# Kernel optimization log

Measured on AMD Instinct MI355X. Metric: run time of the kernel, lower is better.

## Reference

```python
import jax, jax.numpy as jnp
import numpy as np

N_NODES = 5000
N_EDGES = 50000
BATCH = 8
SEQ = 12
IN_CH = 2
HID = 64
OUT_CH = 1
K = 3
N_LAYERS = 2


def setup_inputs() -> dict:
    key = jax.random.key(0)
    ks = jax.random.split(key, 20)
    d = {}
    d["x"] = jax.random.normal(ks[0], (BATCH, SEQ, N_NODES, IN_CH), dtype=jnp.float32)
    d["edge_index"] = jax.random.randint(ks[1], (2, N_EDGES), 0, N_NODES, dtype=jnp.int32)

    def w(k, fin):
        return jax.random.normal(k, (2, K, fin, HID), dtype=jnp.float32) * 0.05

    fins = [IN_CH + HID, HID + HID]
    i = 2
    for l in range(N_LAYERS):
        for g in ("z", "r", "h"):
            d["W" + g + str(l)] = w(ks[i], fins[l]); i += 1
            d["b" + g + str(l)] = jnp.zeros((HID,), jnp.float32)
    d["Wo"] = jax.random.normal(ks[i], (HID, OUT_CH), dtype=jnp.float32) * 0.05
    d["bo"] = jnp.zeros((OUT_CH,), jnp.float32)
    return d


def reference(x, edge_index,
              Wz0, bz0, Wr0, br0, Wh0, bh0,
              Wz1, bz1, Wr1, br1, Wh1, bh1,
              Wo, bo):
    B, T, N, _ = x.shape
    src, dst = edge_index[0], edge_index[1]
    ones = jnp.ones(src.shape, x.dtype)
    deg_out = jax.ops.segment_sum(ones, src, num_segments=N)
    deg_in = jax.ops.segment_sum(ones, dst, num_segments=N)
    inv = lambda dgr: jnp.where(dgr > 0, 1.0 / dgr, 0.0)
    norm_out = inv(deg_out)[src]  # [E], 1/deg_out(src)
    norm_in = inv(deg_in)[dst]    # [E], 1/deg_in(dst)

    def prop(X, norm):
        # X: [N, B, F] -> sparse matvec via gather/scatter
        msg = norm[:, None, None] * X[src]
        return jax.ops.segment_sum(msg, dst, num_segments=N)

    def dconv(X, W, b):
        # X: [N, B, Fin]; W: [2, K, Fin, H]; dual-direction Chebyshev diffusion
        H = jnp.einsum('nbf,fh->nbh', X, W[0, 0] + W[1, 0])
        Tx0o = Tx0i = X
        Tx1o = prop(X, norm_out)
        Tx1i = prop(X, norm_in)
        H = H + jnp.einsum('nbf,fh->nbh', Tx1o, W[0, 1]) \
              + jnp.einsum('nbf,fh->nbh', Tx1i, W[1, 1])
        for k in range(2, W.shape[1]):
            Tx2o = 2.0 * prop(Tx1o, norm_out) - Tx0o
            Tx2i = 2.0 * prop(Tx1i, norm_in) - Tx0i
            H = H + jnp.einsum('nbf,fh->nbh', Tx2o, W[0, k]) \
                  + jnp.einsum('nbf,fh->nbh', Tx2i, W[1, k])
            Tx0o, Tx1o = Tx1o, Tx2o
            Tx0i, Tx1i = Tx1i, Tx2i
        return H + b

    def cell(Xin, H, p):
        Wz, bz, Wr, br, Wh, bh = p
        XH = jnp.concatenate([Xin, H], axis=-1)
        Z = jax.nn.sigmoid(dconv(XH, Wz, bz))
        R = jax.nn.sigmoid(dconv(XH, Wr, br))
        Ht = jnp.tanh(dconv(jnp.concatenate([Xin, H * R], axis=-1), Wh, bh))
        return Z * H + (1.0 - Z) * Ht

    layers = [(Wz0, bz0, Wr0, br0, Wh0, bh0), (Wz1, bz1, Wr1, br1, Wh1, bh1)]
    hid = Wo.shape[0]
    h0 = jnp.zeros((len(layers), N, B, hid), x.dtype)
    xs = jnp.transpose(x, (1, 2, 0, 3))  # [T, N, B, F]

    def step(h, xt):
        inp = xt
        new_h = []
        for l, p in enumerate(layers):
            hl = cell(inp, h[l], p)
            new_h.append(hl)
            inp = hl
        h = jnp.stack(new_h)
        out = jnp.einsum('nbh,ho->nbo', h[-1], Wo) + bo
        return h, out

    _, outs = jax.lax.scan(step, h0, xs)      # [T, N, B, O]
    return jnp.transpose(outs, (2, 0, 1, 3))  # [B, T, N, O]
```

## Files before the change

### kernel.cpp

```cpp
#include <hip/hip_runtime.h>
#include <math.h>

#define NNODES 5000
#define NEDGES 50000
#define SEQT 12
#define NB 40000
#define MAXDEG 128

typedef __attribute__((ext_vector_type(8))) _Float16 half8;
typedef __attribute__((ext_vector_type(2))) _Float16 half2v;
typedef __attribute__((ext_vector_type(4))) float f32x4;


__global__ void count_deg_k(const int* __restrict__ ei, int* deg_out, int* deg_in){
    int e = blockIdx.x*blockDim.x + threadIdx.x;
    if (e < NEDGES){
        atomicAdd(&deg_out[ei[e]], 1);
        atomicAdd(&deg_in[ei[NEDGES + e]], 1);
    }
}

__global__ void scan_k(const int* __restrict__ deg_in, int* __restrict__ row_ptr){
    __shared__ int part[256];
    int tid = threadIdx.x;
    int base = tid*20;
    int loc[20]; int s = 0;
    for (int i=0;i<20;i++){
        int idx = base+i;
        int v = (idx < NNODES) ? deg_in[idx] : 0;
        loc[i] = s; s += v;
    }
    part[tid] = s;
    __syncthreads();
    for (int off=1; off<256; off<<=1){
        int v = (tid>=off) ? part[tid-off] : 0;
        __syncthreads();
        part[tid] += v;
        __syncthreads();
    }
    int prev = (tid==0) ? 0 : part[tid-1];
    for (int i=0;i<20;i++){
        int idx = base+i;
        if (idx < NNODES) row_ptr[idx] = prev + loc[i];
    }
    if (tid==255) row_ptr[NNODES] = part[255];
}

__global__ void fill_csr_k(const int* __restrict__ ei, const int* __restrict__ deg_out,
                           const int* __restrict__ deg_in, const int* __restrict__ row_ptr,
                           int* cursor, int* __restrict__ csr_src,
                           float* __restrict__ csr_wo, float* __restrict__ csr_wi){
    int e = blockIdx.x*blockDim.x + threadIdx.x;
    if (e >= NEDGES) return;
    int s = ei[e], d = ei[NEDGES+e];
    int pos = atomicAdd(&cursor[d], 1);
    int slot = row_ptr[d] + pos;
    csr_src[slot] = s;
    csr_wo[slot] = 1.f/(float)deg_out[s];
    csr_wi[slot] = 1.f/(float)deg_in[d];
}

__global__ void prepack_x_k(const float* __restrict__ x, _Float16* __restrict__ Xtph){
    int idx = blockIdx.x*256 + threadIdx.x;
    if (idx >= SEQT*NB*2) return;
    int tt = idx / (NB*2);
    int r2 = idx - tt*(NB*2);
    int row = r2 >> 1, f = r2 & 1;
    int n = row >> 3, b = row & 7;
    Xtph[idx] = (_Float16)x[((size_t)(b*SEQT+tt)*NNODES + n)*2 + f];
}

__device__ __forceinline__ float wfetch(const float* __restrict__ W, int F, int slot, int f, int c){
    const float* p0 = W + ((size_t)0*F + f)*64 + c;
    const float* p1 = W + ((size_t)1*F + f)*64 + c;
    const float* p2 = W + ((size_t)2*F + f)*64 + c;
    const float* p3 = W + ((size_t)3*F + f)*64 + c;
    const float* p4 = W + ((size_t)4*F + f)*64 + c;
    const float* p5 = W + ((size_t)5*F + f)*64 + c;
    switch(slot){
        case 0: return *p0 + *p3 - *p2 - *p5;
        case 1: return *p1;
        case 2: return *p4;
        case 3: return 2.f * *p2;
        default: return 2.f * *p5;
    }
}

__global__ void pack_l0_k(const float* __restrict__ W, _Float16* __restrict__ wh){
    int idx = blockIdx.x*256 + threadIdx.x;
    if (idx >= 4*11*64) return;
    int lane = idx & 63, rest = idx >> 6;
    int ks = rest % 11, cf = rest / 11;
    int col = cf*16 + (lane & 15);
    int kb = ks*32 + ((lane>>4)<<3);
    size_t o = ((size_t)(ks*4 + cf)*64 + lane)*8;
    for (int j=0;j<8;j++){
        int k = kb + j;
        float v = 0.f;
        if (ks == 0){
            if (k < 10) v = wfetch(W, 66, k>>1, k&1, col);
        } else {
            int slot = (ks-1)>>1;
            int f = 2 + k - 32 - 64*slot;
            v = wfetch(W, 66, slot, f, col);
        }
        wh[o+j] = (_Float16)v;
    }
}

__global__ void pack_l1_k(const float* __restrict__ W, _Float16* __restrict__ wh){
    int idx = blockIdx.x*256 + threadIdx.x;
    if (idx >= 4*20*64) return;
    int lane = idx & 63, rest = idx >> 6;
    int ks = rest % 20, cf = rest / 20;
    int col = cf*16 + (lane & 15);
    int kb = ks*32 + ((lane>>4)<<3);
    int slot = ks >> 2;
    size_t o = ((size_t)(ks*4 + cf)*64 + lane)*8;
    for (int j=0;j<8;j++){
        int k = kb + j;
        int f = k - slot*128;
        wh[o+j] = (_Float16)wfetch(W, 128, slot, f, col);
    }
}


__global__ __launch_bounds__(128) void k_f1(int aCount,
    const _Float16* __restrict__ h0h, const _Float16* __restrict__ h1h,
    _Float16* __restrict__ T1o128, _Float16* __restrict__ T1i128,
    const _Float16* __restrict__ Xt,
    _Float16* __restrict__ Th1o, _Float16* __restrict__ Th1i, _Float16* __restrict__ XTh,
    const int* __restrict__ rp, const int* __restrict__ cs,
    const float* __restrict__ cwo, const float* __restrict__ cwi){
    __shared__ int s_o[MAXDEG]; __shared__ float swo[MAXDEG], swi[MAXDEG];
    const int bx = blockIdx.x;
    const bool isA = bx < aCount;
    const int n = isA ? bx : bx - aCount;
    int beg = rp[n], deg = rp[n+1]-beg;
    int nst = deg < MAXDEG ? deg : MAXDEG;
    for (int j=threadIdx.x; j<nst; j+=128){
        s_o[j] = cs[beg+j]*512;
        swo[j] = cwo[beg+j]; swi[j] = cwi[beg+j];
    }
    __syncthreads();
    if (isA){
        int off = threadIdx.x*8;
        int b = off >> 7, c = off & 127;
        const _Float16* S = (c < 64) ? h0h : h1h;
        int soff = b*64 + (c & 63);
        float ao[8] = {0,0,0,0,0,0,0,0}, ai[8] = {0,0,0,0,0,0,0,0};
        for (int j=0;j<nst;j++){
            half8 v = *(const half8*)(S + s_o[j] + soff);
            float wo=swo[j], wi=swi[j];
            #pragma unroll
            for (int e=0;e<8;e++){
                float xv = (float)v[e];
                ao[e]=fmaf(wo,xv,ao[e]); ai[e]=fmaf(wi,xv,ai[e]);
            }
        }
        for (int j=nst;j<deg;j++){
            half8 v = *(const half8*)(S + (size_t)cs[beg+j]*512 + soff);
            float wo=cwo[beg+j], wi=cwi[beg+j];
            #pragma unroll
            for (int e=0;e<8;e++){
                float xv = (float)v[e];
                ao[e]=fmaf(wo,xv,ao[e]); ai[e]=fmaf(wi,xv,ai[e]);
            }
        }
        half8 po, pi;
        #pragma unroll
        for (int e=0;e<8;e++){ po[e]=(_Float16)ao[e]; pi[e]=(_Float16)ai[e]; }
        *(half8*)(T1o128 + (size_t)n*1024 + off) = po;
        *(half8*)(T1i128 + (size_t)n*1024 + off) = pi;
    } else {
        if (threadIdx.x < 64){
            int off = threadIdx.x*8;
            float ao[8] = {0,0,0,0,0,0,0,0}, ai[8] = {0,0,0,0,0,0,0,0};
            for (int j=0;j<nst;j++){
                half8 v = *(const half8*)(h0h + s_o[j] + off);
                float wo=swo[j], wi=swi[j];
                #pragma unroll
                for (int e=0;e<8;e++){
                    float xv = (float)v[e];
                    ao[e]=fmaf(wo,xv,ao[e]); ai[e]=fmaf(wi,xv,ai[e]);
                }
            }
            for (int j=nst;j<deg;j++){
                half8 v = *(const half8*)(h0h + (size_t)cs[beg+j]*512 + off);
                float wo=cwo[beg+j], wi=cwi[beg+j];
                #pragma unroll
                for (int e=0;e<8;e++){
                    float xv = (float)v[e];
                    ao[e]=fmaf(wo,xv,ao[e]); ai[e]=fmaf(wi,xv,ai[e]);
                }
            }
            half8 po, pi;
            #pragma unroll
            for (int e=0;e<8;e++){ po[e]=(_Float16)ao[e]; pi[e]=(_Float16)ai[e]; }
            *(half8*)(Th1o + (size_t)n*512 + off) = po;
            *(half8*)(Th1i + (size_t)n*512 + off) = pi;
        }
        if (threadIdx.x < 8){
            int b = threadIdx.x;
            float ax0=0,ax1=0, ay0=0,ay1=0;
            for (int j=0;j<nst;j++){
                int src = s_o[j] >> 9;
                half2v v = *(const half2v*)(Xt + src*16 + b*2);
                float x0=(float)v[0], x1=(float)v[1];
                ax0=fmaf(swo[j],x0,ax0); ax1=fmaf(swo[j],x1,ax1);
                ay0=fmaf(swi[j],x0,ay0); ay1=fmaf(swi[j],x1,ay1);
            }
            for (int j=nst;j<deg;j++){
                int src = cs[beg+j];
                half2v v = *(const half2v*)(Xt + src*16 + b*2);
                float x0=(float)v[0], x1=(float)v[1];
                ax0=fmaf(cwo[beg+j],x0,ax0); ax1=fmaf(cwo[beg+j],x1,ax1);
                ay0=fmaf(cwi[beg+j],x0,ay0); ay1=fmaf(cwi[beg+j],x1,ay1);
            }
            size_t ro = (size_t)(n*8 + b)*32;
            XTh[ro+0] = Xt[(size_t)(n*8+b)*2+0];
            XTh[ro+1] = Xt[(size_t)(n*8+b)*2+1];
            XTh[ro+2] = (_Float16)ax0; XTh[ro+3] = (_Float16)ax1;
            XTh[ro+4] = (_Float16)ay0; XTh[ro+5] = (_Float16)ay1;
        }
    }
}

__global__ __launch_bounds__(128) void k_f2(int aCount,
    const _Float16* __restrict__ T1o128, const _Float16* __restrict__ T1i128,
    _Float16* __restrict__ U2o128, _Float16* __restrict__ U2i128,
    const _Float16* __restrict__ Th1o, const _Float16* __restrict__ Th1i,
    _Float16* __restrict__ Th2o, _Float16* __restrict__ Th2i, _Float16* __restrict__ XTh,
    const int* __restrict__ rp, const int* __restrict__ cs,
    const float* __restrict__ cwo, const float* __restrict__ cwi){
    __shared__ int s_o[MAXDEG]; __shared__ float s_w[MAXDEG];
    const int bx = blockIdx.x;
    const bool isA = bx < aCount;
    const int idx = isA ? bx : bx - aCount;
    const int n = idx >> 1, sel = idx & 1;
    const float* cw = sel ? cwi : cwo;
    int beg = rp[n], deg = rp[n+1]-beg;
    int nst = deg < MAXDEG ? deg : MAXDEG;
    const int scale = isA ? 1024 : 512;
    for (int j=threadIdx.x; j<nst; j+=128){
        s_o[j] = cs[beg+j]*scale;
        s_w[j] = cw[beg+j];
    }
    __syncthreads();
    if (isA){
        const _Float16* S = sel ? T1i128 : T1o128;
        _Float16* U = sel ? U2i128 : U2o128;
        int off = threadIdx.x*8;
        float a[8] = {0,0,0,0,0,0,0,0};
        for (int j=0;j<nst;j++){
            half8 v = *(const half8*)(S + s_o[j] + off);
            float w=s_w[j];
            #pragma unroll
            for (int e=0;e<8;e++) a[e]=fmaf(w,(float)v[e],a[e]);
        }
        for (int j=nst;j<deg;j++){
            half8 v = *(const half8*)(S + (size_t)cs[beg+j]*1024 + off);
            float w=cw[beg+j];
            #pragma unroll
            for (int e=0;e<8;e++) a[e]=fmaf(w,(float)v[e],a[e]);
        }
        half8 p;
        #pragma unroll
        for (int e=0;e<8;e++) p[e]=(_Float16)a[e];
        *(half8*)(U + (size_t)n*1024 + off) = p;
    } else {
        const _Float16* S = sel ? Th1i : Th1o;
        _Float16* U = sel ? Th2i : Th2o;
        if (threadIdx.x < 64){
            int off = threadIdx.x*8;
            float a[8] = {0,0,0,0,0,0,0,0};
            for (int j=0;j<nst;j++){
                half8 v = *(const half8*)(S + s_o[j] + off);
                float w=s_w[j];
                #pragma unroll
                for (int e=0;e<8;e++) a[e]=fmaf(w,(float)v[e],a[e]);
            }
            for (int j=nst;j<deg;j++){
                half8 v = *(const half8*)(S + (size_t)cs[beg+j]*512 + off);
                float w=cw[beg+j];
                #pragma unroll
                for (int e=0;e<8;e++) a[e]=fmaf(w,(float)v[e],a[e]);
            }
            half8 p;
            #pragma unroll
            for (int e=0;e<8;e++) p[e]=(_Float16)a[e];
            *(half8*)(U + (size_t)n*512 + off) = p;
        }
        if (threadIdx.x < 8){
            int b = threadIdx.x;
            int xo = 2 + 2*sel;
            float a0=0,a1=0;
            for (int j=0;j<nst;j++){
                int src = s_o[j] >> 9;
                half2v v = *(const half2v*)(XTh + (size_t)src*256 + b*32 + xo);
                a0=fmaf(s_w[j],(float)v[0],a0); a1=fmaf(s_w[j],(float)v[1],a1);
            }
            for (int j=nst;j<deg;j++){
                int src = cs[beg+j];
                float w = cw[beg+j];
                half2v v = *(const half2v*)(XTh + (size_t)src*256 + b*32 + xo);
                a0=fmaf(w,(float)v[0],a0); a1=fmaf(w,(float)v[1],a1);
            }
            size_t ro = (size_t)(n*8 + b)*32 + 6 + 2*sel;
            XTh[ro+0] = (_Float16)a0; XTh[ro+1] = (_Float16)a1;
        }
    }
}

__global__ __launch_bounds__(64) void k_f4(int aCount,
    const _Float16* __restrict__ SA, _Float16* __restrict__ YoA, _Float16* __restrict__ YiA,
    const _Float16* __restrict__ SB, _Float16* __restrict__ YoB, _Float16* __restrict__ YiB,
    const int* __restrict__ rp, const int* __restrict__ cs,
    const float* __restrict__ cwo, const float* __restrict__ cwi){
    __shared__ int s_o[MAXDEG]; __shared__ float swo[MAXDEG], swi[MAXDEG];
    const int bx = blockIdx.x;
    const bool isA = bx < aCount;
    const int n = isA ? bx : bx - aCount;
    const _Float16* S = isA ? SA : SB;
    _Float16* Yo = isA ? YoA : YoB;
    _Float16* Yi = isA ? YiA : YiB;
    int beg = rp[n], deg = rp[n+1]-beg;
    int nst = deg < MAXDEG ? deg : MAXDEG;
    for (int j=threadIdx.x; j<nst; j+=64){
        s_o[j] = cs[beg+j]*512;
        swo[j] = cwo[beg+j]; swi[j] = cwi[beg+j];
    }
    __syncthreads();
    int off = threadIdx.x*8;
    float ao[8] = {0,0,0,0,0,0,0,0}, ai[8] = {0,0,0,0,0,0,0,0};
    for (int j=0;j<nst;j++){
        half8 v = *(const half8*)(S + s_o[j] + off);
        float wo=swo[j], wi=swi[j];
        #pragma unroll
        for (int e=0;e<8;e++){
            float xv = (float)v[e];
            ao[e]=fmaf(wo,xv,ao[e]); ai[e]=fmaf(wi,xv,ai[e]);
        }
    }
    for (int j=nst;j<deg;j++){
        half8 v = *(const half8*)(S + (size_t)cs[beg+j]*512 + off);
        float wo=cwo[beg+j], wi=cwi[beg+j];
        #pragma unroll
        for (int e=0;e<8;e++){
            float xv = (float)v[e];
            ao[e]=fmaf(wo,xv,ao[e]); ai[e]=fmaf(wi,xv,ai[e]);
        }
    }
    half8 po, pi;
    #pragma unroll
    for (int e=0;e<8;e++){ po[e]=(_Float16)ao[e]; pi[e]=(_Float16)ai[e]; }
    *(half8*)(Yo + (size_t)n*512 + off) = po;
    *(half8*)(Yi + (size_t)n*512 + off) = pi;
}

__global__ __launch_bounds__(64) void k_f5(int aCount,
    const _Float16* __restrict__ T1oA, const _Float16* __restrict__ T1iA,
    _Float16* __restrict__ U2oA, _Float16* __restrict__ U2iA,
    const _Float16* __restrict__ T1oB, const _Float16* __restrict__ T1iB,
    _Float16* __restrict__ U2oB, _Float16* __restrict__ U2iB,
    const int* __restrict__ rp, const int* __restrict__ cs,
    const float* __restrict__ cwo, const float* __restrict__ cwi){
    __shared__ int s_o[MAXDEG]; __shared__ float s_w[MAXDEG];
    const int bx = blockIdx.x;
    const bool isA = bx < aCount;
    const int idx = isA ? bx : bx - aCount;
    const int n = idx >> 1, sel = idx & 1;
    const _Float16* S = isA ? (sel ? T1iA : T1oA) : (sel ? T1iB : T1oB);
    _Float16* U = isA ? (sel ? U2iA : U2oA) : (sel ? U2iB : U2oB);
    const float* cw = sel ? cwi : cwo;
    int beg = rp[n], deg = rp[n+1]-beg;
    int nst = deg < MAXDEG ? deg : MAXDEG;
    for (int j=threadIdx.x; j<nst; j+=64){
        s_o[j] = cs[beg+j]*512;
        s_w[j] = cw[beg+j];
    }
    __syncthreads();
    int off = threadIdx.x*8;
    float a[8] = {0,0,0,0,0,0,0,0};
    for (int j=0;j<nst;j++){
        half8 v = *(const half8*)(S + s_o[j] + off);
        float w=s_w[j];
        #pragma unroll
        for (int e=0;e<8;e++) a[e]=fmaf(w,(float)v[e],a[e]);
    }
    for (int j=nst;j<deg;j++){
        half8 v = *(const half8*)(S + (size_t)cs[beg+j]*512 + off);
        float w=cw[beg+j];
        #pragma unroll
        for (int e=0;e<8;e++) a[e]=fmaf(w,(float)v[e],a[e]);
    }
    half8 p;
    #pragma unroll
    for (int e=0;e<8;e++) p[e]=(_Float16)a[e];
    *(half8*)(U + (size_t)n*512 + off) = p;
}


struct KD { const _Float16* a; int st; };
struct GA { KD kd[20]; };

template<int NK, int NG, int EPI>
__device__ __forceinline__ void gemm_body(char* smemraw, int bxm, const GA& ga,
    const _Float16* __restrict__ wh0, const float* __restrict__ b0,
    const _Float16* __restrict__ wh1, const float* __restrict__ b1,
    float* __restrict__ Z, _Float16* __restrict__ Gout,
    float* __restrict__ Hf, _Float16* __restrict__ Hh,
    const float* __restrict__ Wo, const float* __restrict__ bo,
    float* __restrict__ out, int t){
    _Float16* ldsb = (_Float16*)smemraw;
    float* spr = (float*)(smemraw + (size_t)4*NG*2048);
    const int tid = threadIdx.x;
    const int lane = tid & 63, wv = tid >> 6, rl = lane & 15, kg = lane >> 4;
    const int m0 = bxm*64 + (wv&1)*32;
    const int cfb = (wv>>1)*2;
    const _Float16* wsrc[2] = {wh0, wh1};

    half8 srg[NG];
    half8 a0, a1, a0n, a1n;

    auto sload = [&](int ks){
        #pragma unroll
        for (int j=0;j<NG;j++)
            srg[j] = *(const half8*)(wsrc[j] + (size_t)ks*2048 + tid*8);
    };
    auto swrite = [&](int buf){
        #pragma unroll
        for (int j=0;j<NG;j++)
            *(half8*)&ldsb[buf*(NG*2048) + j*2048 + tid*8] = srg[j];
    };
    auto aload = [&](int ks, half8& x0, half8& x1){
        const _Float16* base = ga.kd[ks].a;
        const int st = ga.kd[ks].st;
        x0 = *(const half8*)(base + (size_t)(m0+rl)*st + kg*8);
        x1 = *(const half8*)(base + (size_t)(m0+16+rl)*st + kg*8);
    };

    f32x4 acc[NG][2][2];
    #pragma unroll
    for (int g=0; g<NG; ++g)
        #pragma unroll
        for (int cc=0; cc<2; ++cc)
            #pragma unroll
            for (int mr=0; mr<2; ++mr){
                acc[g][cc][mr][0]=0.f; acc[g][cc][mr][1]=0.f;
                acc[g][cc][mr][2]=0.f; acc[g][cc][mr][3]=0.f;
            }

    sload(0); swrite(0);
    if (NK>1) sload(1);
    aload(0, a0, a1);
    __syncthreads();
    for (int ks=0; ks<NK; ++ks){
        const int cur = ks & 1;
        if (ks+1 < NK){ swrite(cur^1); aload(ks+1, a0n, a1n); }
        if (ks+2 < NK) sload(ks+2);
        #pragma unroll
        for (int g=0; g<NG; ++g){
            #pragma unroll
            for (int cc=0; cc<2; ++cc){
                half8 bv = *(const half8*)&ldsb[cur*(NG*2048) + g*2048 + (cfb+cc)*512 + lane*8];
                acc[g][cc][0] = __builtin_amdgcn_mfma_f32_16x16x32_f16(a0, bv, acc[g][cc][0], 0, 0, 0);
                acc[g][cc][1] = __builtin_amdgcn_mfma_f32_16x16x32_f16(a1, bv, acc[g][cc][1], 0, 0, 0);
            }
        }
        __syncthreads();
        a0 = a0n; a1 = a1n;
    }

    if constexpr (EPI == 0){
        #pragma unroll
        for (int cc=0; cc<2; ++cc){
            const int col = (cfb+cc)*16 + rl;
            float bzv = b0[col], brv = b1[col];
            #pragma unroll
            for (int mr=0; mr<2; ++mr)
                #pragma unroll
                for (int i=0;i<4;i++){
                    int row = m0 + mr*16 + kg*4 + i;
                    float z = 1.f/(1.f+__expf(-(acc[0][cc][mr][i] + bzv)));
                    float r = 1.f/(1.f+__expf(-(acc[NG-1][cc][mr][i] + brv)));
                    size_t ix = (size_t)row*64 + col;
                    Z[ix] = z;
                    Gout[ix] = (_Float16)(Hf[ix]*r);
                }
        }
    } else {
        float pr[2][4] = {{0.f,0.f,0.f,0.f},{0.f,0.f,0.f,0.f}};
        #pragma unroll
        for (int cc=0; cc<2; ++cc){
            const int col = (cfb+cc)*16 + rl;
            float bv = b0[col];
            float wo_c = 0.f;
            if constexpr (EPI == 2) wo_c = Wo[col];
            #pragma unroll
            for (int mr=0; mr<2; ++mr)
                #pragma unroll
                for (int i=0;i<4;i++){
                    int row = m0 + mr*16 + kg*4 + i;
                    float ht = tanhf(acc[0][cc][mr][i] + bv);
                    size_t ix = (size_t)row*64 + col;
                    float z = Z[ix];
                    float hn = z*Hf[ix] + (1.f-z)*ht;
                    Hf[ix] = hn;
                    Hh[ix] = (_Float16)hn;
                    if constexpr (EPI == 2) pr[mr][i] = fmaf(hn, wo_c, pr[mr][i]);
                }
        }
        if constexpr (EPI == 2){
            #pragma unroll
            for (int mr=0; mr<2; ++mr)
                #pragma unroll
                for (int i=0;i<4;i++){
                    float v = pr[mr][i];
                    v += __shfl_xor(v, 1);
                    v += __shfl_xor(v, 2);
                    v += __shfl_xor(v, 4);
                    v += __shfl_xor(v, 8);
                    if (rl == 0) spr[wv*32 + mr*16 + kg*4 + i] = v;
                }
            __syncthreads();
            if (tid < 64){
                int r = tid;
                float v = spr[(r>>5)*32 + (r&31)] + spr[((r>>5)|2)*32 + (r&31)] + bo[0];
                int row = bxm*64 + r;
                int n = row >> 3, b = row & 7;
                out[(size_t)(b*SEQT + t)*NNODES + n] = v;
            }
        }
    }
}

__global__ __launch_bounds__(256) void k_f3(int aCount,
    GA gaA, const _Float16* whA0, const float* bA0, const _Float16* whA1, const float* bA1,
    float* ZA, _Float16* GoA, float* HfA,
    GA gaB, const _Float16* whB0, const float* bB0, const _Float16* whB1, const float* bB1,
    float* ZB, _Float16* GoB, float* HfB){
    __shared__ __align__(16) char smem[4*2*2048 + 512];
    if (blockIdx.x < aCount)
        gemm_body<20,2,0>(smem, blockIdx.x, gaA, whA0, bA0, whA1, bA1,
                          ZA, GoA, HfA, nullptr, nullptr, nullptr, nullptr, 0);
    else
        gemm_body<11,2,0>(smem, blockIdx.x - aCount, gaB, whB0, bB0, whB1, bB1,
                          ZB, GoB, HfB, nullptr, nullptr, nullptr, nullptr, 0);
}

__global__ __launch_bounds__(256) void k_f6(int aCount,
    GA gaA, const _Float16* whA, const float* bA,
    float* ZA, float* HfA, _Float16* HhA,
    const float* Wo, const float* bo, float* out, int t,
    GA gaB, const _Float16* whB, const float* bB,
    float* ZB, float* HfB, _Float16* HhB){
    __shared__ __align__(16) char smem[4*1*2048 + 512];
    if (blockIdx.x < aCount)
        gemm_body<20,1,2>(smem, blockIdx.x, gaA, whA, bA, nullptr, nullptr,
                          ZA, nullptr, HfA, HhA, Wo, bo, out, t);
    else
        gemm_body<11,1,1>(smem, blockIdx.x - aCount, gaB, whB, bB, nullptr, nullptr,
                          ZB, nullptr, HfB, HhB, nullptr, nullptr, nullptr, 0);
}


extern "C" void kernel_launch(void* const* d_in, const int* in_sizes, int n_in,
                              void* d_out, int out_size, void* d_ws, size_t ws_size,
                              hipStream_t stream){
    (void)in_sizes; (void)n_in; (void)out_size; (void)ws_size;
    const float* x  = (const float*)d_in[0];
    const int*   ei = (const int*)d_in[1];
    const float* Wz[2] = {(const float*)d_in[2],  (const float*)d_in[8]};
    const float* bz[2] = {(const float*)d_in[3],  (const float*)d_in[9]};
    const float* Wr[2] = {(const float*)d_in[4],  (const float*)d_in[10]};
    const float* br[2] = {(const float*)d_in[5],  (const float*)d_in[11]};
    const float* Wh[2] = {(const float*)d_in[6],  (const float*)d_in[12]};
    const float* bh[2] = {(const float*)d_in[7],  (const float*)d_in[13]};
    const float* Wo = (const float*)d_in[14];
    const float* bo = (const float*)d_in[15];
    float* out = (float*)d_out;

    char* p = (char*)d_ws;
    auto alloc = [&](size_t bytes)->char*{
        char* r = p; p += (bytes + 255) & ~(size_t)255; return r;
    };
    const size_t H64  = (size_t)NB*64*2;
    const size_t H128 = (size_t)NB*128*2;
    const size_t F64  = (size_t)NB*64*4;

    _Float16* Xtph = (_Float16*)alloc((size_t)SEQT*NB*2*2);
    float*    h0f = (float*)alloc(F64);
    float*    h1f = (float*)alloc(F64);
    float*    Z0  = (float*)alloc(F64);
    float*    Z1  = (float*)alloc(F64);
    _Float16* h0hb[2];
    h0hb[0] = (_Float16*)alloc(H64);
    h0hb[1] = (_Float16*)alloc(H64);
    _Float16* h1h = (_Float16*)alloc(H64);
    _Float16* XTh = (_Float16*)alloc((size_t)NB*32*2);
    _Float16* Th1o = (_Float16*)alloc(H64);
    _Float16* Th1i = (_Float16*)alloc(H64);
    _Float16* Th2o = (_Float16*)alloc(H64);
    _Float16* Th2i = (_Float16*)alloc(H64);
    _Float16* G0L0 = (_Float16*)alloc(H64);
    _Float16* G1o0 = (_Float16*)alloc(H64);
    _Float16* G1i0 = (_Float16*)alloc(H64);
    _Float16* G2o0 = (_Float16*)alloc(H64);
    _Float16* G2i0 = (_Float16*)alloc(H64);
    _Float16* T1o128 = (_Float16*)alloc(H128);
    _Float16* T1i128 = (_Float16*)alloc(H128);
    _Float16* U2o128 = (_Float16*)alloc(H128);
    _Float16* U2i128 = (_Float16*)alloc(H128);
    _Float16* G0p  = (_Float16*)alloc(H64);
    _Float16* G1o1 = (_Float16*)alloc(H64);
    _Float16* G1i1 = (_Float16*)alloc(H64);
    _Float16* G2o1 = (_Float16*)alloc(H64);
    _Float16* G2i1 = (_Float16*)alloc(H64);
    _Float16 *whl0[3], *whl1[3];
    for (int g=0; g<3; ++g){
        whl0[g] = (_Float16*)alloc((size_t)4*11*64*8*2);
        whl1[g] = (_Float16*)alloc((size_t)4*20*64*8*2);
    }
    int* deg_out = (int*)alloc(NNODES*4);
    int* deg_in  = (int*)alloc(NNODES*4);
    int* row_ptr = (int*)alloc((NNODES+1)*4);
    int* cursor  = (int*)alloc(NNODES*4);
    int* csr_src = (int*)alloc(NEDGES*4);
    float* csr_wo = (float*)alloc(NEDGES*4);
    float* csr_wi = (float*)alloc(NEDGES*4);

    hipMemsetAsync(deg_out, 0, NNODES*4, stream);
    hipMemsetAsync(deg_in,  0, NNODES*4, stream);
    hipMemsetAsync(cursor,  0, NNODES*4, stream);
    hipMemsetAsync(h0f, 0, F64, stream);
    hipMemsetAsync(h1f, 0, F64, stream);
    hipMemsetAsync(h0hb[0], 0, H64, stream);
    hipMemsetAsync(h0hb[1], 0, H64, stream);
    hipMemsetAsync(h1h, 0, H64, stream);
    hipMemsetAsync(XTh, 0, (size_t)NB*32*2, stream);

    count_deg_k<<<(NEDGES+255)/256, 256, 0, stream>>>(ei, deg_out, deg_in);
    scan_k<<<1, 256, 0, stream>>>(deg_in, row_ptr);
    fill_csr_k<<<(NEDGES+255)/256, 256, 0, stream>>>(ei, deg_out, deg_in, row_ptr,
                                                     cursor, csr_src, csr_wo, csr_wi);
    prepack_x_k<<<(SEQT*NB*2+255)/256, 256, 0, stream>>>(x, Xtph);
    const float* Wptr0[3] = {Wz[0], Wr[0], Wh[0]};
    const float* Wptr1[3] = {Wz[1], Wr[1], Wh[1]};
    for (int g=0; g<3; ++g){
        pack_l0_k<<<(4*11*64+255)/256, 256, 0, stream>>>(Wptr0[g], whl0[g]);
        pack_l1_k<<<(4*20*64+255)/256, 256, 0, stream>>>(Wptr1[g], whl1[g]);
    }

    GA gaL0zr[2] = {}, gaL1zr[2] = {}, gaL1h[2] = {}, gaL0h = {};
    for (int pp=0; pp<2; ++pp){
        const _Float16* t64[5] = {h0hb[pp], Th1o, Th1i, Th2o, Th2i};
        gaL0zr[pp].kd[0] = {XTh, 32};
        for (int s=0; s<5; ++s){
            gaL0zr[pp].kd[1+2*s] = {t64[s], 64};
            gaL0zr[pp].kd[2+2*s] = {t64[s]+32, 64};
        }
        gaL1zr[pp].kd[0] = {h0hb[pp], 64};    gaL1zr[pp].kd[1] = {h0hb[pp]+32, 64};
        gaL1zr[pp].kd[2] = {h1h, 64};         gaL1zr[pp].kd[3] = {h1h+32, 64};
        const _Float16* t128[4] = {T1o128, T1i128, U2o128, U2i128};
        for (int s=0; s<4; ++s)
            for (int q=0; q<4; ++q)
                gaL1zr[pp].kd[4+4*s+q] = {t128[s]+32*q, 128};
        gaL1h[pp].kd[0] = {h0hb[pp], 64};  gaL1h[pp].kd[1] = {h0hb[pp]+32, 64};
        gaL1h[pp].kd[2] = {G0p, 64};       gaL1h[pp].kd[3] = {G0p+32, 64};
        const _Float16* gh[4] = {G1o1, G1i1, G2o1, G2i1};
        for (int s=0; s<4; ++s){
            gaL1h[pp].kd[4+4*s+0] = {t128[s], 128};
            gaL1h[pp].kd[4+4*s+1] = {t128[s]+32, 128};
            gaL1h[pp].kd[4+4*s+2] = {gh[s], 64};
            gaL1h[pp].kd[4+4*s+3] = {gh[s]+32, 64};
        }
    }
    {
        const _Float16* g64[5] = {G0L0, G1o0, G1i0, G2o0, G2i0};
        gaL0h.kd[0] = {XTh, 32};
        for (int s=0; s<5; ++s){
            gaL0h.kd[1+2*s] = {g64[s], 64};
            gaL0h.kd[2+2*s] = {g64[s]+32, 64};
        }
    }

    k_f1<<<NNODES, 128, 0, stream>>>(0, h0hb[1], h1h, T1o128, T1i128,
        Xtph, Th1o, Th1i, XTh, row_ptr, csr_src, csr_wo, csr_wi);
    k_f2<<<2*NNODES, 128, 0, stream>>>(0, T1o128, T1i128, U2o128, U2i128,
        Th1o, Th1i, Th2o, Th2i, XTh, row_ptr, csr_src, csr_wo, csr_wi);
    k_f3<<<625, 256, 0, stream>>>(0,
        gaL1zr[1], whl1[0], bz[1], whl1[1], br[1], Z1, G0p, h1f,
        gaL0zr[1], whl0[0], bz[0], whl0[1], br[0], Z0, G0L0, h0f);
    k_f4<<<NNODES, 64, 0, stream>>>(0, G0p, G1o1, G1i1, G0L0, G1o0, G1i0,
        row_ptr, csr_src, csr_wo, csr_wi);
    k_f5<<<2*NNODES, 64, 0, stream>>>(0, G1o1, G1i1, G2o1, G2i1,
        G1o0, G1i0, G2o0, G2i0, row_ptr, csr_src, csr_wo, csr_wi);
    k_f6<<<625, 256, 0, stream>>>(0,
        gaL1h[1], whl1[2], bh[1], Z1, h1f, h1h, Wo, bo, out, 0,
        gaL0h, whl0[2], bh[0], Z0, h0f, h0hb[0]);

    for (int s=0; s<SEQT; ++s){
        const int pr = s & 1;
        const int doB = (s+1 < SEQT) ? 1 : 0;
        k_f1<<<NNODES*(1+doB), 128, 0, stream>>>(NNODES,
            h0hb[pr], h1h, T1o128, T1i128,
            Xtph + (size_t)(doB ? s+1 : s)*NB*2, Th1o, Th1i, XTh,
            row_ptr, csr_src, csr_wo, csr_wi);
        k_f2<<<2*NNODES*(1+doB), 128, 0, stream>>>(2*NNODES,
            T1o128, T1i128, U2o128, U2i128,
            Th1o, Th1i, Th2o, Th2i, XTh, row_ptr, csr_src, csr_wo, csr_wi);
        k_f3<<<625*(1+doB), 256, 0, stream>>>(625,
            gaL1zr[pr], whl1[0], bz[1], whl1[1], br[1], Z1, G0p, h1f,
            gaL0zr[pr], whl0[0], bz[0], whl0[1], br[0], Z0, G0L0, h0f);
        k_f4<<<NNODES*(1+doB), 64, 0, stream>>>(NNODES,
            G0p, G1o1, G1i1, G0L0, G1o0, G1i0, row_ptr, csr_src, csr_wo, csr_wi);
        k_f5<<<2*NNODES*(1+doB), 64, 0, stream>>>(2*NNODES,
            G1o1, G1i1, G2o1, G2i1, G1o0, G1i0, G2o0, G2i0,
            row_ptr, csr_src, csr_wo, csr_wi);
        k_f6<<<625*(1+doB), 256, 0, stream>>>(625,
            gaL1h[pr], whl1[2], bh[1], Z1, h1f, h1h, Wo, bo, out, s,
            gaL0h, whl0[2], bh[0], Z0, h0f, h0hb[(s+1)&1]);
    }
}
```

Measured before the change: 2.178 ms.

## Reuse layer-0 hidden-state diffusion for layer-1 input instead of re-propagating it

The layer-1 first-stage blocks previously diffused the 128-channel concatenation [h0,h1]. Layer-0 blocks already diffuse the same h0 for the next step's layer 0. Now layer-1 blocks diffuse only h1 into 64-channel buffers, and the layer-1 GEMM operand tables read the h0 half from the shared Th1o/Th1i/Th2o/Th2i buffers. This is meant to remove roughly a third of the sparse gather traffic in the two propagation kernels. Block size drops to 64 threads. The B half now also runs on the last step, because layer 1 depends on its output.

```diff
diff --git a/kernel.cpp b/kernel.cpp
--- a/kernel.cpp
+++ b/kernel.cpp
@@ -125,9 +125,9 @@
 }
 
 
-__global__ __launch_bounds__(128) void k_f1(int aCount,
+__global__ __launch_bounds__(64) void k_f1(int aCount,
     const _Float16* __restrict__ h0h, const _Float16* __restrict__ h1h,
-    _Float16* __restrict__ T1o128, _Float16* __restrict__ T1i128,
+    _Float16* __restrict__ T1o64, _Float16* __restrict__ T1i64,
     const _Float16* __restrict__ Xt,
     _Float16* __restrict__ Th1o, _Float16* __restrict__ Th1i, _Float16* __restrict__ XTh,
     const int* __restrict__ rp, const int* __restrict__ cs,
@@ -138,19 +138,19 @@
     const int n = isA ? bx : bx - aCount;
     int beg = rp[n], deg = rp[n+1]-beg;
     int nst = deg < MAXDEG ? deg : MAXDEG;
-    for (int j=threadIdx.x; j<nst; j+=128){
+    for (int j=threadIdx.x; j<nst; j+=64){
         s_o[j] = cs[beg+j]*512;
         swo[j] = cwo[beg+j]; swi[j] = cwi[beg+j];
     }
     __syncthreads();
-    if (isA){
-        int off = threadIdx.x*8;
-        int b = off >> 7, c = off & 127;
-        const _Float16* S = (c < 64) ? h0h : h1h;
-        int soff = b*64 + (c & 63);
+    const _Float16* S = isA ? h1h : h0h;
+    _Float16* Yo = isA ? T1o64 : Th1o;
+    _Float16* Yi = isA ? T1i64 : Th1i;
+    int off = threadIdx.x*8;
+    {
         float ao[8] = {0,0,0,0,0,0,0,0}, ai[8] = {0,0,0,0,0,0,0,0};
         for (int j=0;j<nst;j++){
-            half8 v = *(const half8*)(S + s_o[j] + soff);
+            half8 v = *(const half8*)(S + s_o[j] + off);
             float wo=swo[j], wi=swi[j];
             #pragma unroll
             for (int e=0;e<8;e++){
@@ -159,7 +159,7 @@
             }
         }
         for (int j=nst;j<deg;j++){
-            half8 v = *(const half8*)(S + (size_t)cs[beg+j]*512 + soff);
+            half8 v = *(const half8*)(S + (size_t)cs[beg+j]*512 + off);
             float wo=cwo[beg+j], wi=cwi[beg+j];
             #pragma unroll
             for (int e=0;e<8;e++){
@@ -170,65 +170,37 @@
         half8 po, pi;
         #pragma unroll
         for (int e=0;e<8;e++){ po[e]=(_Float16)ao[e]; pi[e]=(_Float16)ai[e]; }
-        *(half8*)(T1o128 + (size_t)n*1024 + off) = po;
-        *(half8*)(T1i128 + (size_t)n*1024 + off) = pi;
-    } else {
-        if (threadIdx.x < 64){
-            int off = threadIdx.x*8;
-            float ao[8] = {0,0,0,0,0,0,0,0}, ai[8] = {0,0,0,0,0,0,0,0};
-            for (int j=0;j<nst;j++){
-                half8 v = *(const half8*)(h0h + s_o[j] + off);
-                float wo=swo[j], wi=swi[j];
-                #pragma unroll
-                for (int e=0;e<8;e++){
-                    float xv = (float)v[e];
-                    ao[e]=fmaf(wo,xv,ao[e]); ai[e]=fmaf(wi,xv,ai[e]);
-                }
-            }
-            for (int j=nst;j<deg;j++){
-                half8 v = *(const half8*)(h0h + (size_t)cs[beg+j]*512 + off);
-                float wo=cwo[beg+j], wi=cwi[beg+j];
-                #pragma unroll
-                for (int e=0;e<8;e++){
-                    float xv = (float)v[e];
-                    ao[e]=fmaf(wo,xv,ao[e]); ai[e]=fmaf(wi,xv,ai[e]);
-                }
-            }
-            half8 po, pi;
-            #pragma unroll
-            for (int e=0;e<8;e++){ po[e]=(_Float16)ao[e]; pi[e]=(_Float16)ai[e]; }
-            *(half8*)(Th1o + (size_t)n*512 + off) = po;
-            *(half8*)(Th1i + (size_t)n*512 + off) = pi;
-        }
-        if (threadIdx.x < 8){
-            int b = threadIdx.x;
-            float ax0=0,ax1=0, ay0=0,ay1=0;
-            for (int j=0;j<nst;j++){
-                int src = s_o[j] >> 9;
-                half2v v = *(const half2v*)(Xt + src*16 + b*2);
-                float x0=(float)v[0], x1=(float)v[1];
-                ax0=fmaf(swo[j],x0,ax0); ax1=fmaf(swo[j],x1,ax1);
-                ay0=fmaf(swi[j],x0,ay0); ay1=fmaf(swi[j],x1,ay1);
-            }
-            for (int j=nst;j<deg;j++){
-                int src = cs[beg+j];
-                half2v v = *(const half2v*)(Xt + src*16 + b*2);
-                float x0=(float)v[0], x1=(float)v[1];
-                ax0=fmaf(cwo[beg+j],x0,ax0); ax1=fmaf(cwo[beg+j],x1,ax1);
-                ay0=fmaf(cwi[beg+j],x0,ay0); ay1=fmaf(cwi[beg+j],x1,ay1);
-            }
-            size_t ro = (size_t)(n*8 + b)*32;
-            XTh[ro+0] = Xt[(size_t)(n*8+b)*2+0];
-            XTh[ro+1] = Xt[(size_t)(n*8+b)*2+1];
-            XTh[ro+2] = (_Float16)ax0; XTh[ro+3] = (_Float16)ax1;
-            XTh[ro+4] = (_Float16)ay0; XTh[ro+5] = (_Float16)ay1;
-        }
-    }
-}
-
-__global__ __launch_bounds__(128) void k_f2(int aCount,
-    const _Float16* __restrict__ T1o128, const _Float16* __restrict__ T1i128,
-    _Float16* __restrict__ U2o128, _Float16* __restrict__ U2i128,
+        *(half8*)(Yo + (size_t)n*512 + off) = po;
+        *(half8*)(Yi + (size_t)n*512 + off) = pi;
+    }
+    if (!isA && threadIdx.x < 8){
+        int b = threadIdx.x;
+        float ax0=0,ax1=0, ay0=0,ay1=0;
+        for (int j=0;j<nst;j++){
+            int src = s_o[j] >> 9;
+            half2v v = *(const half2v*)(Xt + src*16 + b*2);
+            float x0=(float)v[0], x1=(float)v[1];
+            ax0=fmaf(swo[j],x0,ax0); ax1=fmaf(swo[j],x1,ax1);
+            ay0=fmaf(swi[j],x0,ay0); ay1=fmaf(swi[j],x1,ay1);
+        }
+        for (int j=nst;j<deg;j++){
+            int src = cs[beg+j];
+            half2v v = *(const half2v*)(Xt + src*16 + b*2);
+            float x0=(float)v[0], x1=(float)v[1];
+            ax0=fmaf(cwo[beg+j],x0,ax0); ax1=fmaf(cwo[beg+j],x1,ax1);
+            ay0=fmaf(cwi[beg+j],x0,ay0); ay1=fmaf(cwi[beg+j],x1,ay1);
+        }
+        size_t ro = (size_t)(n*8 + b)*32;
+        XTh[ro+0] = Xt[(size_t)(n*8+b)*2+0];
+        XTh[ro+1] = Xt[(size_t)(n*8+b)*2+1];
+        XTh[ro+2] = (_Float16)ax0; XTh[ro+3] = (_Float16)ax1;
+        XTh[ro+4] = (_Float16)ay0; XTh[ro+5] = (_Float16)ay1;
+    }
+}
+
+__global__ __launch_bounds__(64) void k_f2(int aCount,
+    const _Float16* __restrict__ T1o64, const _Float16* __restrict__ T1i64,
+    _Float16* __restrict__ U2o64, _Float16* __restrict__ U2i64,
     const _Float16* __restrict__ Th1o, const _Float16* __restrict__ Th1i,
     _Float16* __restrict__ Th2o, _Float16* __restrict__ Th2i, _Float16* __restrict__ XTh,
     const int* __restrict__ rp, const int* __restrict__ cs,
@@ -241,16 +213,15 @@
     const float* cw = sel ? cwi : cwo;
     int beg = rp[n], deg = rp[n+1]-beg;
     int nst = deg < MAXDEG ? deg : MAXDEG;
-    const int scale = isA ? 1024 : 512;
-    for (int j=threadIdx.x; j<nst; j+=128){
-        s_o[j] = cs[beg+j]*scale;
+    for (int j=threadIdx.x; j<nst; j+=64){
+        s_o[j] = cs[beg+j]*512;
         s_w[j] = cw[beg+j];
     }
     __syncthreads();
-    if (isA){
-        const _Float16* S = sel ? T1i128 : T1o128;
-        _Float16* U = sel ? U2i128 : U2o128;
-        int off = threadIdx.x*8;
+    const _Float16* S = isA ? (sel ? T1i64 : T1o64) : (sel ? Th1i : Th1o);
+    _Float16* U = isA ? (sel ? U2i64 : U2o64) : (sel ? Th2i : Th2o);
+    int off = threadIdx.x*8;
+    {
         float a[8] = {0,0,0,0,0,0,0,0};
         for (int j=0;j<nst;j++){
             half8 v = *(const half8*)(S + s_o[j] + off);
@@ -259,7 +230,7 @@
             for (int e=0;e<8;e++) a[e]=fmaf(w,(float)v[e],a[e]);
         }
         for (int j=nst;j<deg;j++){
-            half8 v = *(const half8*)(S + (size_t)cs[beg+j]*1024 + off);
+            half8 v = *(const half8*)(S + (size_t)cs[beg+j]*512 + off);
             float w=cw[beg+j];
             #pragma unroll
             for (int e=0;e<8;e++) a[e]=fmaf(w,(float)v[e],a[e]);
@@ -267,48 +238,25 @@
         half8 p;
         #pragma unroll
         for (int e=0;e<8;e++) p[e]=(_Float16)a[e];
-        *(half8*)(U + (size_t)n*1024 + off) = p;
-    } else {
-        const _Float16* S = sel ? Th1i : Th1o;
-        _Float16* U = sel ? Th2i : Th2o;
-        if (threadIdx.x < 64){
-            int off = threadIdx.x*8;
-            float a[8] = {0,0,0,0,0,0,0,0};
-            for (int j=0;j<nst;j++){
-                half8 v = *(const half8*)(S + s_o[j] + off);
-                float w=s_w[j];
-                #pragma unroll
-                for (int e=0;e<8;e++) a[e]=fmaf(w,(float)v[e],a[e]);
-            }
-            for (int j=nst;j<deg;j++){
-                half8 v = *(const half8*)(S + (size_t)cs[beg+j]*512 + off);
-                float w=cw[beg+j];
-                #pragma unroll
-                for (int e=0;e<8;e++) a[e]=fmaf(w,(float)v[e],a[e]);
-            }
-            half8 p;
-            #pragma unroll
-            for (int e=0;e<8;e++) p[e]=(_Float16)a[e];
-            *(half8*)(U + (size_t)n*512 + off) = p;
-        }
-        if (threadIdx.x < 8){
-            int b = threadIdx.x;
-            int xo = 2 + 2*sel;
-            float a0=0,a1=0;
-            for (int j=0;j<nst;j++){
-                int src = s_o[j] >> 9;
-                half2v v = *(const half2v*)(XTh + (size_t)src*256 + b*32 + xo);
-                a0=fmaf(s_w[j],(float)v[0],a0); a1=fmaf(s_w[j],(float)v[1],a1);
-            }
-            for (int j=nst;j<deg;j++){
-                int src = cs[beg+j];
-                float w = cw[beg+j];
-                half2v v = *(const half2v*)(XTh + (size_t)src*256 + b*32 + xo);
-                a0=fmaf(w,(float)v[0],a0); a1=fmaf(w,(float)v[1],a1);
-            }
-            size_t ro = (size_t)(n*8 + b)*32 + 6 + 2*sel;
-            XTh[ro+0] = (_Float16)a0; XTh[ro+1] = (_Float16)a1;
-        }
+        *(half8*)(U + (size_t)n*512 + off) = p;
+    }
+    if (!isA && threadIdx.x < 8){
+        int b = threadIdx.x;
+        int xo = 2 + 2*sel;
+        float a0=0,a1=0;
+        for (int j=0;j<nst;j++){
+            int src = s_o[j] >> 9;
+            half2v v = *(const half2v*)(XTh + (size_t)src*256 + b*32 + xo);
+            a0=fmaf(s_w[j],(float)v[0],a0); a1=fmaf(s_w[j],(float)v[1],a1);
+        }
+        for (int j=nst;j<deg;j++){
+            int src = cs[beg+j];
+            float w = cw[beg+j];
+            half2v v = *(const half2v*)(XTh + (size_t)src*256 + b*32 + xo);
+            a0=fmaf(w,(float)v[0],a0); a1=fmaf(w,(float)v[1],a1);
+        }
+        size_t ro = (size_t)(n*8 + b)*32 + 6 + 2*sel;
+        XTh[ro+0] = (_Float16)a0; XTh[ro+1] = (_Float16)a1;
     }
 }
 
@@ -586,7 +534,6 @@
         char* r = p; p += (bytes + 255) & ~(size_t)255; return r;
     };
     const size_t H64  = (size_t)NB*64*2;
-    const size_t H128 = (size_t)NB*128*2;
     const size_t F64  = (size_t)NB*64*4;
 
     _Float16* Xtph = (_Float16*)alloc((size_t)SEQT*NB*2*2);
@@ -608,10 +555,10 @@
     _Float16* G1i0 = (_Float16*)alloc(H64);
     _Float16* G2o0 = (_Float16*)alloc(H64);
     _Float16* G2i0 = (_Float16*)alloc(H64);
-    _Float16* T1o128 = (_Float16*)alloc(H128);
-    _Float16* T1i128 = (_Float16*)alloc(H128);
-    _Float16* U2o128 = (_Float16*)alloc(H128);
-    _Float16* U2i128 = (_Float16*)alloc(H128);
+    _Float16* T1o64 = (_Float16*)alloc(H64);
+    _Float16* T1i64 = (_Float16*)alloc(H64);
+    _Float16* U2o64 = (_Float16*)alloc(H64);
+    _Float16* U2i64 = (_Float16*)alloc(H64);
     _Float16* G0p  = (_Float16*)alloc(H64);
     _Float16* G1o1 = (_Float16*)alloc(H64);
     _Float16* G1i1 = (_Float16*)alloc(H64);
@@ -653,6 +600,8 @@
     }
 
     GA gaL0zr[2] = {}, gaL1zr[2] = {}, gaL1h[2] = {}, gaL0h = {};
+    const _Float16* hsrc[4] = {Th1o, Th1i, Th2o, Th2i};
+    const _Float16* g64s[4] = {T1o64, T1i64, U2o64, U2i64};
     for (int pp=0; pp<2; ++pp){
         const _Float16* t64[5] = {h0hb[pp], Th1o, Th1i, Th2o, Th2i};
         gaL0zr[pp].kd[0] = {XTh, 32};
@@ -662,16 +611,18 @@
         }
         gaL1zr[pp].kd[0] = {h0hb[pp], 64};    gaL1zr[pp].kd[1] = {h0hb[pp]+32, 64};
         gaL1zr[pp].kd[2] = {h1h, 64};         gaL1zr[pp].kd[3] = {h1h+32, 64};
-        const _Float16* t128[4] = {T1o128, T1i128, U2o128, U2i128};
-        for (int s=0; s<4; ++s)
-            for (int q=0; q<4; ++q)
-                gaL1zr[pp].kd[4+4*s+q] = {t128[s]+32*q, 128};
+        for (int s=0; s<4; ++s){
+            gaL1zr[pp].kd[4+4*s+0] = {hsrc[s], 64};
+            gaL1zr[pp].kd[4+4*s+1] = {hsrc[s]+32, 64};
+            gaL1zr[pp].kd[4+4*s+2] = {g64s[s], 64};
+            gaL1zr[pp].kd[4+4*s+3] = {g64s[s]+32, 64};
+        }
         gaL1h[pp].kd[0] = {h0hb[pp], 64};  gaL1h[pp].kd[1] = {h0hb[pp]+32, 64};
         gaL1h[pp].kd[2] = {G0p, 64};       gaL1h[pp].kd[3] = {G0p+32, 64};
         const _Float16* gh[4] = {G1o1, G1i1, G2o1, G2i1};
         for (int s=0; s<4; ++s){
-            gaL1h[pp].kd[4+4*s+0] = {t128[s], 128};
-            gaL1h[pp].kd[4+4*s+1] = {t128[s]+32, 128};
+            gaL1h[pp].kd[4+4*s+0] = {hsrc[s], 64};
+            gaL1h[pp].kd[4+4*s+1] = {hsrc[s]+32, 64};
             gaL1h[pp].kd[4+4*s+2] = {gh[s], 64};
             gaL1h[pp].kd[4+4*s+3] = {gh[s]+32, 64};
         }
@@ -685,9 +636,9 @@
         }
     }
 
-    k_f1<<<NNODES, 128, 0, stream>>>(0, h0hb[1], h1h, T1o128, T1i128,
+    k_f1<<<NNODES, 64, 0, stream>>>(0, h0hb[1], h1h, T1o64, T1i64,
         Xtph, Th1o, Th1i, XTh, row_ptr, csr_src, csr_wo, csr_wi);
-    k_f2<<<2*NNODES, 128, 0, stream>>>(0, T1o128, T1i128, U2o128, U2i128,
+    k_f2<<<2*NNODES, 64, 0, stream>>>(0, T1o64, T1i64, U2o64, U2i64,
         Th1o, Th1i, Th2o, Th2i, XTh, row_ptr, csr_src, csr_wo, csr_wi);
     k_f3<<<625, 256, 0, stream>>>(0,
         gaL1zr[1], whl1[0], bz[1], whl1[1], br[1], Z1, G0p, h1f,
@@ -703,12 +654,12 @@
     for (int s=0; s<SEQT; ++s){
         const int pr = s & 1;
         const int doB = (s+1 < SEQT) ? 1 : 0;
-        k_f1<<<NNODES*(1+doB), 128, 0, stream>>>(NNODES,
-            h0hb[pr], h1h, T1o128, T1i128,
-            Xtph + (size_t)(doB ? s+1 : s)*NB*2, Th1o, Th1i, XTh,
+        const _Float16* xp = Xtph + (size_t)(doB ? s+1 : s)*NB*2;
+        k_f1<<<2*NNODES, 64, 0, stream>>>(NNODES,
+            h0hb[pr], h1h, T1o64, T1i64, xp, Th1o, Th1i, XTh,
             row_ptr, csr_src, csr_wo, csr_wi);
-        k_f2<<<2*NNODES*(1+doB), 128, 0, stream>>>(2*NNODES,
-            T1o128, T1i128, U2o128, U2i128,
+        k_f2<<<4*NNODES, 64, 0, stream>>>(2*NNODES,
+            T1o64, T1i64, U2o64, U2i64,
             Th1o, Th1i, Th2o, Th2i, XTh, row_ptr, csr_src, csr_wo, csr_wi);
         k_f3<<<625*(1+doB), 256, 0, stream>>>(625,
             gaL1zr[pr], whl1[0], bz[1], whl1[1], br[1], Z1, G0p, h1f,
```

Measured after the change: 1.947 ms. 10.6% less time.
